# Kernel tuning notes

Measured on AMD Instinct MI355X. Metric: run time of the kernel, lower is better.

## Reference

```python
import jax, jax.numpy as jnp
import numpy as np

S, B, GL, OL = 512, 2048, 32, 20      # leaves: count, batch, genes, out
M, C, GM, OM = 32, 16, 64, 20         # mids: count, children, genes, out
GR, OR = 128, 38                      # root genes, root out
IM = C * OL + GM                      # 384 mid input
IR = M * OM + GR                      # 768 root input
EPS = 1e-5


def _bn(h, g, be, axis):
    # training-mode BatchNorm1d: biased batch variance, eps=1e-5
    m = h.mean(axis=axis, keepdims=True)
    v = h.var(axis=axis, keepdims=True)
    return g * (h - m) * jax.lax.rsqrt(v + EPS) + be


def setup_inputs() -> dict:
    key = jax.random.key(0)
    ks = jax.random.split(key, 8)
    d = {
        'x_leaf': jax.random.uniform(ks[0], (S, B, GL), dtype=jnp.float32),
        'x_mid': jax.random.uniform(ks[1], (M, B, GM), dtype=jnp.float32),
        'x_root': jax.random.uniform(ks[2], (B, GR), dtype=jnp.float32),
        'W_leaf': jax.random.normal(ks[3], (S, GL, OL), dtype=jnp.float32) * 0.1,
        'b_leaf': jnp.zeros((S, OL), jnp.float32),
        'g_leaf': jnp.ones((S, OL), jnp.float32),
        'be_leaf': jnp.zeros((S, OL), jnp.float32),
        'W_mid': jax.random.normal(ks[4], (M, IM, OM), dtype=jnp.float32) * 0.05,
        'b_mid': jnp.zeros((M, OM), jnp.float32),
        'g_mid': jnp.ones((M, OM), jnp.float32),
        'be_mid': jnp.zeros((M, OM), jnp.float32),
        'W_root': jax.random.normal(ks[5], (IR, OR), dtype=jnp.float32) * 0.05,
        'b_root': jnp.zeros((OR,), jnp.float32),
        'g_root': jnp.ones((OR,), jnp.float32),
        'be_root': jnp.zeros((OR,), jnp.float32),
    }
    return d


def reference(x_leaf, x_mid, x_root, W_leaf, b_leaf, g_leaf, be_leaf,
              W_mid, b_mid, g_mid, be_mid, W_root, b_root, g_root, be_root):
    # --- leaf subsystems (grouped GEMM over 512 subsystems) ---
    h = jnp.tanh(jnp.einsum('sbi,sio->sbo', x_leaf, W_leaf) + b_leaf[:, None, :])
    leaf_out = _bn(h, g_leaf[:, None, :], be_leaf[:, None, :], 1)  # [S,B,OL]
    # --- mid subsystems: concat(genes, child outputs) ---
    child = leaf_out.reshape(M, C, B, OL).transpose(0, 2, 1, 3).reshape(M, B, C * OL)
    xm = jnp.concatenate([x_mid, child], axis=-1)  # [M,B,IM]
    h = jnp.tanh(jnp.einsum('mbi,mio->mbo', xm, W_mid) + b_mid[:, None, :])
    mid_out = _bn(h, g_mid[:, None, :], be_mid[:, None, :], 1)  # [M,B,OM]
    # --- root subsystem ---
    childr = mid_out.transpose(1, 0, 2).reshape(B, M * OM)
    xr = jnp.concatenate([x_root, childr], axis=-1)  # [B,IR]
    h = jnp.tanh(xr @ W_root + b_root)
    return _bn(h, g_root, be_root, 0)  # [B,OR]
```

## Files before the change

kernel.cpp:

```cpp
#include <hip/hip_runtime.h>
#include <hip/hip_bf16.h>

#define SS 512
#define BATCH 2048
#define GL 32
#define OL 20
#define MM 32
#define CC 16
#define GM 64
#define OM 20
#define GR 128
#define ORR 38
#define IMID 384
#define IROOT 768
#define EPSBN 1e-5f

#define KSPLIT 16
#define KCH 48

#define SZ_CHILD ((size_t)SS * OL * BATCH)
#define OFF_SCL  (SZ_CHILD)
#define OFF_SHL  (OFF_SCL + (size_t)SS * OL)
#define OFF_HM   (OFF_SHL + (size_t)SS * OL)
#define OFF_MP   (OFF_HM + (size_t)MM * OM * BATCH)
#define OFF_HR   (OFF_MP + (size_t)MM * 32 * 2 * OM)
#define OFF_RP   (OFF_HR + (size_t)BATCH * ORR)
#define OFF_SCM  (OFF_RP + (size_t)32 * 76)
#define OFF_SHM  (OFF_SCM + (size_t)MM * OM)
#define OFF_PW   (OFF_SHM + (size_t)MM * OM)
#define OFF_LP   (OFF_PW + (size_t)KSPLIT * BATCH * ORR)

__device__ __forceinline__ float tanh_fast(float x) {
  float ax = fabsf(x);
  float e  = __expf(-2.0f * ax);
  float r  = __fdividef(1.0f - e, 1.0f + e);
  return copysignf(r, x);
}

__device__ __forceinline__ unsigned short f2bf(float f) {
  unsigned u = __builtin_bit_cast(unsigned, f);
  return (unsigned short)((u + 0x7FFFu + ((u >> 16) & 1u)) >> 16);
}

typedef __attribute__((ext_vector_type(8))) short short8v;
typedef __attribute__((ext_vector_type(4))) float f32x4;

#define FMA20(xs, wptr, acc) do { \
  const float4* _wr = (const float4*)(wptr); \
  float4 _w0=_wr[0], _w1=_wr[1], _w2=_wr[2], _w3=_wr[3], _w4=_wr[4]; \
  acc[0]=fmaf(xs,_w0.x,acc[0]);  acc[1]=fmaf(xs,_w0.y,acc[1]); \
  acc[2]=fmaf(xs,_w0.z,acc[2]);  acc[3]=fmaf(xs,_w0.w,acc[3]); \
  acc[4]=fmaf(xs,_w1.x,acc[4]);  acc[5]=fmaf(xs,_w1.y,acc[5]); \
  acc[6]=fmaf(xs,_w1.z,acc[6]);  acc[7]=fmaf(xs,_w1.w,acc[7]); \
  acc[8]=fmaf(xs,_w2.x,acc[8]);  acc[9]=fmaf(xs,_w2.y,acc[9]); \
  acc[10]=fmaf(xs,_w2.z,acc[10]); acc[11]=fmaf(xs,_w2.w,acc[11]); \
  acc[12]=fmaf(xs,_w3.x,acc[12]); acc[13]=fmaf(xs,_w3.y,acc[13]); \
  acc[14]=fmaf(xs,_w3.z,acc[14]); acc[15]=fmaf(xs,_w3.w,acc[15]); \
  acc[16]=fmaf(xs,_w4.x,acc[16]); acc[17]=fmaf(xs,_w4.y,acc[17]); \
  acc[18]=fmaf(xs,_w4.z,acc[18]); acc[19]=fmaf(xs,_w4.w,acc[19]); \
} while (0)

__global__ __launch_bounds__(256) void k_leaf(
    const float* __restrict__ x, const float* __restrict__ W,
    const float* __restrict__ bias, float* __restrict__ child,
    float* __restrict__ lp)
{
  const int chunk = blockIdx.x;
  const int s = blockIdx.y;
  const int t = threadIdx.x;
  const int w = t >> 6, l = t & 63;
  const int col = l & 15;
  const int kb = (l >> 4) * 8;

  __shared__ float hb[OL * 260];
  __shared__ float Wl[GL * OL];
  __shared__ float bl[OL];
  __shared__ float red[4][2 * OL];

  if (t < GL * OL / 4)
    ((float4*)Wl)[t] = ((const float4*)(W + (size_t)s * GL * OL))[t];
  else if (t >= 160 && t < 165)
    ((float4*)bl)[t - 160] = ((const float4*)(bias + s * OL))[t - 160];
  __syncthreads();

  short8v b0, b1;
#pragma unroll
  for (int j = 0; j < 8; j++) {
    const int k = kb + j;
    b0[j] = (short)f2bf(Wl[k * OL + col]);
    b1[j] = (col < 4) ? (short)f2bf(Wl[k * OL + 16 + col]) : (short)0;
  }
  const float blv0 = bl[col];
  const float blv1 = (col < 4) ? bl[16 + col] : 0.f;

  float sum0 = 0.f, ssq0 = 0.f, sum1 = 0.f, ssq1 = 0.f;
  const f32x4 zero = {0.f, 0.f, 0.f, 0.f};

#pragma unroll
  for (int T = 0; T < 4; T++) {
    const int tl = T * 64 + w * 16;
    const int row_g = chunk * 256 + tl + col;
    const float4* xr = (const float4*)(x + ((size_t)s * BATCH + row_g) * GL + kb);
    float4 v0 = xr[0], v1 = xr[1];
    short8v a;
    a[0] = (short)f2bf(v0.x); a[1] = (short)f2bf(v0.y);
    a[2] = (short)f2bf(v0.z); a[3] = (short)f2bf(v0.w);
    a[4] = (short)f2bf(v1.x); a[5] = (short)f2bf(v1.y);
    a[6] = (short)f2bf(v1.z); a[7] = (short)f2bf(v1.w);

    f32x4 d0 = __builtin_amdgcn_mfma_f32_16x16x32_bf16(a, b0, zero, 0, 0, 0);
    f32x4 d1 = __builtin_amdgcn_mfma_f32_16x16x32_bf16(a, b1, zero, 0, 0, 0);

    const int rowloc = tl + (l >> 4) * 4;
    float4 o0;
    o0.x = tanh_fast(d0[0] + blv0); o0.y = tanh_fast(d0[1] + blv0);
    o0.z = tanh_fast(d0[2] + blv0); o0.w = tanh_fast(d0[3] + blv0);
    sum0 += o0.x + o0.y + o0.z + o0.w;
    ssq0 = fmaf(o0.x, o0.x, fmaf(o0.y, o0.y, fmaf(o0.z, o0.z, fmaf(o0.w, o0.w, ssq0))));
    *(float4*)&hb[col * 260 + rowloc] = o0;
    if (col < 4) {
      float4 o1;
      o1.x = tanh_fast(d1[0] + blv1); o1.y = tanh_fast(d1[1] + blv1);
      o1.z = tanh_fast(d1[2] + blv1); o1.w = tanh_fast(d1[3] + blv1);
      sum1 += o1.x + o1.y + o1.z + o1.w;
      ssq1 = fmaf(o1.x, o1.x, fmaf(o1.y, o1.y, fmaf(o1.z, o1.z, fmaf(o1.w, o1.w, ssq1))));
      *(float4*)&hb[(16 + col) * 260 + rowloc] = o1;
    }
  }
  __syncthreads();

#pragma unroll
  for (int j = 0; j < 5; j++) {
    const int f = t + j * 256;
    const int plane = f >> 6, q = (f & 63) * 4;
    float4 v = *(const float4*)&hb[plane * 260 + q];
    *(float4*)&child[((size_t)s * OL + plane) * BATCH + chunk * 256 + q] = v;
  }

  sum0 += __shfl_xor(sum0, 16); sum0 += __shfl_xor(sum0, 32);
  ssq0 += __shfl_xor(ssq0, 16); ssq0 += __shfl_xor(ssq0, 32);
  sum1 += __shfl_xor(sum1, 16); sum1 += __shfl_xor(sum1, 32);
  ssq1 += __shfl_xor(ssq1, 16); ssq1 += __shfl_xor(ssq1, 32);
  if (l < 16) { red[w][l] = sum0; red[w][OL + l] = ssq0; }
  if (l < 4)  { red[w][16 + l] = sum1; red[w][OL + 16 + l] = ssq1; }
  __syncthreads();
  if (t < 2 * OL) {
    float v = red[0][t] + red[1][t] + red[2][t] + red[3][t];
    lp[((size_t)s * 8 + chunk) * (2 * OL) + t] = v;
  }
}

__global__ __launch_bounds__(256) void k_leafstats(
    const float* __restrict__ lp, const float* __restrict__ g,
    const float* __restrict__ be,
    float* __restrict__ scL, float* __restrict__ shL)
{
  const int e = blockIdx.x * 256 + threadIdx.x;
  if (e >= SS * OL) return;
  const int s = e / OL, o = e % OL;
  float s1 = 0.f, s2 = 0.f;
#pragma unroll
  for (int c = 0; c < 8; c++) {
    s1 += lp[((size_t)s * 8 + c) * (2 * OL) + o];
    s2 += lp[((size_t)s * 8 + c) * (2 * OL) + OL + o];
  }
  float mean = s1 * (1.f / BATCH);
  float var  = s2 * (1.f / BATCH) - mean * mean;
  float rs = rsqrtf(var + EPSBN);
  float sc = g[e] * rs;
  scL[e] = sc;
  shL[e] = be[e] - mean * sc;
}

__global__ __launch_bounds__(256, 2) void k_mid(
    const float* __restrict__ xg, const float* __restrict__ child,
    const float* __restrict__ scL, const float* __restrict__ shL,
    const float* __restrict__ W, const float* __restrict__ bias,
    float* __restrict__ hm, float* __restrict__ mp)
{
  const int chunk = blockIdx.x;
  const int m = blockIdx.y;
  const int t = threadIdx.x;
  const int kq = t >> 6;
  const int lane = t & 63;
  const int b = chunk * 64 + lane;

  __shared__ float Wl[IMID * OM];
  __shared__ float cb[3][64][21];
  __shared__ float scs[CC * OL];
  __shared__ float shs[CC * OL];
  __shared__ float xgb[64 * 69];

  for (int i = t; i < IMID * OM / 4; i += 256)
    ((float4*)Wl)[i] = ((const float4*)(W + (size_t)m * IMID * OM))[i];
  if (t < 80)       ((float4*)scs)[t]      = ((const float4*)(scL + m * CC * OL))[t];
  else if (t < 160) ((float4*)shs)[t - 80] = ((const float4*)(shL + m * CC * OL))[t - 80];

  {
    const float4* gs = (const float4*)(xg + ((size_t)m * BATCH + chunk * 64) * GM);
#pragma unroll
    for (int j = 0; j < 4; j++) {
      const int f = t + j * 256;
      float4 v = gs[f];
      const int r = f >> 4, c4 = (f & 15) << 2;
      float* wp = &xgb[r * 69 + c4];
      wp[0] = v.x; wp[1] = v.y; wp[2] = v.z; wp[3] = v.w;
    }
  }
  __syncthreads();

  float acc[OM];
#pragma unroll
  for (int o = 0; o < OM; o++) acc[o] = 0.f;

  const float* grow = &xgb[lane * 69 + kq * 16];
#pragma unroll
  for (int k = 0; k < 16; k++) {
    FMA20(grow[k], &Wl[(kq * 16 + k) * OM], acc);
  }
#pragma unroll 1
  for (int ci = 0; ci < 4; ci++) {
    const int c = kq * 4 + ci;
    const float* cbase = child + ((size_t)(m * CC + c) * OL) * BATCH + b;
#pragma unroll
    for (int o = 0; o < OL; o++) {
      float v = cbase[(size_t)o * BATCH];
      float xv = fmaf(v, scs[c * OL + o], shs[c * OL + o]);
      FMA20(xv, &Wl[(GM + c * OL + o) * OM], acc);
    }
  }

  if (kq > 0) {
#pragma unroll
    for (int o = 0; o < OM; o++) cb[kq - 1][lane][o] = acc[o];
  }
  __syncthreads();

  if (kq == 0) {
#pragma unroll
    for (int o = 0; o < OM; o++) {
      float v = acc[o] + cb[0][lane][o] + cb[1][lane][o] + cb[2][lane][o] + bias[m * OM + o];
      acc[o] = tanh_fast(v);
    }
#pragma unroll
    for (int o = 0; o < OM; o++)
      hm[((size_t)m * OM + o) * BATCH + b] = acc[o];
#pragma unroll
    for (int o = 0; o < OM; o++) {
      float s1 = acc[o], s2 = acc[o] * acc[o];
#pragma unroll
      for (int d = 32; d >= 1; d >>= 1) { s1 += __shfl_xor(s1, d); s2 += __shfl_xor(s2, d); }
      if (lane == 0) {
        mp[((size_t)m * 32 + chunk) * (2 * OM) + o] = s1;
        mp[((size_t)m * 32 + chunk) * (2 * OM) + OM + o] = s2;
      }
    }
  }
}

__global__ __launch_bounds__(256) void k_midstats(
    const float* __restrict__ mp, const float* __restrict__ g_mid,
    const float* __restrict__ be_mid,
    float* __restrict__ scm, float* __restrict__ shm)
{
  const int e = blockIdx.x * 256 + threadIdx.x;
  if (e >= MM * OM) return;
  const int m = e / OM, o = e % OM;
  float s1 = 0.f, s2 = 0.f;
  for (int c = 0; c < 32; c++) {
    s1 += mp[((size_t)m * 32 + c) * (2 * OM) + o];
    s2 += mp[((size_t)m * 32 + c) * (2 * OM) + OM + o];
  }
  float mean = s1 * (1.f / BATCH);
  float var  = s2 * (1.f / BATCH) - mean * mean;
  float r = rsqrtf(var + EPSBN);
  float sc = g_mid[e] * r;
  scm[e] = sc;
  shm[e] = be_mid[e] - mean * sc;
}

__global__ __launch_bounds__(256, 2) void k_root_partial(
    const float* __restrict__ xr, const float* __restrict__ hm,
    const float* __restrict__ scm, const float* __restrict__ shm,
    const float* __restrict__ W, float* __restrict__ pw)
{
  const int rc = blockIdx.x;
  const int kc = blockIdx.y;
  const int t = threadIdx.x;
  const int w = t >> 6, lane = t & 63;
  const int ob = w * 10;
  const bool full = (w < 3);
  const int b = rc * 64 + lane;
  const int k0 = kc * KCH;

  __shared__ float Wl[KCH * ORR];
  __shared__ float scs[KCH], shs[KCH];

  for (int i = t; i < KCH * ORR; i += 256)
    Wl[i] = W[(size_t)k0 * ORR + i];
  if (t < KCH) {
    const int mi = k0 + t - GR;
    const bool v = (mi >= 0);
    scs[t] = v ? scm[mi] : 0.f;
    shs[t] = v ? shm[mi] : 0.f;
  }
  __syncthreads();

  float acc[10];
#pragma unroll
  for (int j = 0; j < 10; j++) acc[j] = 0.f;

#define FMA10(xs, kk) do { \
    const float2* wr = (const float2*)(Wl + (size_t)(kk) * ORR + ob); \
    float2 w0 = wr[0], w1 = wr[1], w2 = wr[2], w3 = wr[3]; \
    float2 w4 = full ? wr[4] : make_float2(0.f, 0.f); \
    acc[0]=fmaf(xs,w0.x,acc[0]); acc[1]=fmaf(xs,w0.y,acc[1]); \
    acc[2]=fmaf(xs,w1.x,acc[2]); acc[3]=fmaf(xs,w1.y,acc[3]); \
    acc[4]=fmaf(xs,w2.x,acc[4]); acc[5]=fmaf(xs,w2.y,acc[5]); \
    acc[6]=fmaf(xs,w3.x,acc[6]); acc[7]=fmaf(xs,w3.y,acc[7]); \
    acc[8]=fmaf(xs,w4.x,acc[8]); acc[9]=fmaf(xs,w4.y,acc[9]); \
  } while (0)

#pragma unroll 2
  for (int g = 0; g < KCH / 4; g++) {
    const int k = k0 + g * 4;
    float xa[4];
    if (k < GR) {
      float4 xv = *(const float4*)(xr + (size_t)b * GR + k);
      xa[0] = xv.x; xa[1] = xv.y; xa[2] = xv.z; xa[3] = xv.w;
    } else {
      const int mi = k - GR;
      const float* hp = hm + (size_t)mi * BATCH + b;
      const int lk = g * 4;
#pragma unroll
      for (int j = 0; j < 4; j++)
        xa[j] = fmaf(hp[(size_t)j * BATCH], scs[lk + j], shs[lk + j]);
    }
#pragma unroll
    for (int j = 0; j < 4; j++) FMA10(xa[j], g * 4 + j);
  }
#undef FMA10

  const size_t base = ((size_t)kc * BATCH + b) * ORR + ob;
#pragma unroll
  for (int j = 0; j < 10; j++)
    if (j < 8 || full) pw[base + j] = acc[j];
}

__global__ __launch_bounds__(256) void k_rootfinal(
    const float* __restrict__ pw, const float* __restrict__ bias,
    float* __restrict__ hr, float* __restrict__ rp)
{
  const int blk = blockIdx.x;
  const int t = threadIdx.x;
  const int w = t >> 6, lane = t & 63;
  const int ob = w * 10;
  const bool full = (w < 3);
  const int b = blk * 64 + lane;

  float acc[10];
#pragma unroll
  for (int j = 0; j < 10; j++) acc[j] = 0.f;

#pragma unroll 1
  for (int kc = 0; kc < KSPLIT; kc++) {
    const size_t base = ((size_t)kc * BATCH + b) * ORR + ob;
#pragma unroll
    for (int j = 0; j < 10; j++)
      if (j < 8 || full) acc[j] += pw[base + j];
  }

#pragma unroll
  for (int j = 0; j < 10; j++) {
    float bj = (j < 8 || full) ? bias[ob + j] : 0.f;
    acc[j] = tanh_fast(acc[j] + bj);
  }

#pragma unroll
  for (int j = 0; j < 10; j++) {
    float s1 = acc[j], s2 = acc[j] * acc[j];
#pragma unroll
    for (int d = 32; d >= 1; d >>= 1) { s1 += __shfl_xor(s1, d); s2 += __shfl_xor(s2, d); }
    if (lane == 0 && (j < 8 || full)) {
      rp[blk * 76 + ob + j] = s1;
      rp[blk * 76 + ORR + ob + j] = s2;
    }
  }
#pragma unroll
  for (int j = 0; j < 10; j++)
    if (j < 8 || full) hr[(size_t)b * ORR + ob + j] = acc[j];
}

__global__ __launch_bounds__(256) void k_rootnorm(
    const float* __restrict__ hr, const float* __restrict__ rp,
    const float* __restrict__ g, const float* __restrict__ be,
    float* __restrict__ out)
{
  __shared__ float sc[ORR], sh[ORR];
  const int t = threadIdx.x;
  if (t < ORR) {
    float s1 = 0.f, s2 = 0.f;
    for (int blk = 0; blk < 32; blk++) {
      s1 += rp[blk * 76 + t];
      s2 += rp[blk * 76 + ORR + t];
    }
    float mean = s1 * (1.f / BATCH);
    float var  = s2 * (1.f / BATCH) - mean * mean;
    float r = rsqrtf(var + EPSBN);
    float scv = g[t] * r;
    sc[t] = scv;
    sh[t] = be[t] - mean * scv;
  }
  __syncthreads();
  const int idx = blockIdx.x * 256 + t;
  const int o = idx % ORR;
  out[idx] = hr[idx] * sc[o] + sh[o];
}

extern "C" void kernel_launch(void* const* d_in, const int* in_sizes, int n_in,
                              void* d_out, int out_size, void* d_ws, size_t ws_size,
                              hipStream_t stream) {
  (void)in_sizes; (void)n_in; (void)out_size; (void)ws_size;
  const float* x_leaf  = (const float*)d_in[0];
  const float* x_mid   = (const float*)d_in[1];
  const float* x_root  = (const float*)d_in[2];
  const float* W_leaf  = (const float*)d_in[3];
  const float* b_leaf  = (const float*)d_in[4];
  const float* g_leaf  = (const float*)d_in[5];
  const float* be_leaf = (const float*)d_in[6];
  const float* W_mid   = (const float*)d_in[7];
  const float* b_mid   = (const float*)d_in[8];
  const float* g_mid   = (const float*)d_in[9];
  const float* be_mid  = (const float*)d_in[10];
  const float* W_root  = (const float*)d_in[11];
  const float* b_root  = (const float*)d_in[12];
  const float* g_root  = (const float*)d_in[13];
  const float* be_root = (const float*)d_in[14];
  float* out = (float*)d_out;
  float* ws  = (float*)d_ws;

  float* child = ws;
  float* scL   = ws + OFF_SCL;
  float* shL   = ws + OFF_SHL;
  float* hm    = ws + OFF_HM;
  float* mp    = ws + OFF_MP;
  float* hr    = ws + OFF_HR;
  float* rp    = ws + OFF_RP;
  float* scm   = ws + OFF_SCM;
  float* shm   = ws + OFF_SHM;
  float* pw    = ws + OFF_PW;
  float* lp    = ws + OFF_LP;

  k_leaf<<<dim3(8, SS), 256, 0, stream>>>(x_leaf, W_leaf, b_leaf, child, lp);
  k_leafstats<<<40, 256, 0, stream>>>(lp, g_leaf, be_leaf, scL, shL);
  k_mid<<<dim3(32, MM), 256, 0, stream>>>(x_mid, child, scL, shL, W_mid, b_mid,
                                          hm, mp);
  k_midstats<<<3, 256, 0, stream>>>(mp, g_mid, be_mid, scm, shm);
  k_root_partial<<<dim3(32, KSPLIT), 256, 0, stream>>>(x_root, hm, scm, shm,
                                                       W_root, pw);
  k_rootfinal<<<32, 256, 0, stream>>>(pw, b_root, hr, rp);
  k_rootnorm<<<304, 256, 0, stream>>>(hr, rp, g_root, be_root, out);
}
```

Measured before the change: 128.0 us.

## Store leaf outputs and mid weights in bf16, read mid genes directly

Leaf activations are rounded to bf16 before being written to the intermediate child buffer, which halves the bytes written by the leaf kernel and read by the mid kernel. The mid weights are converted to packed bf16 pairs in shared memory, shrinking LDS usage, and the launch-bounds occupancy hint is dropped. Mid gene inputs are now read straight from global memory as float4 instead of being staged through shared memory. This trades accuracy for bandwidth: the leaf BN statistics are still computed from fp32 values, but the activations they normalise are bf16-rounded, and the weights also lose precision.

After: 208.3 us. 62.7% more time.

```diff
diff --git a/kernel.cpp b/kernel.cpp
--- a/kernel.cpp
+++ b/kernel.cpp
@@ -41,28 +41,31 @@
   unsigned u = __builtin_bit_cast(unsigned, f);
   return (unsigned short)((u + 0x7FFFu + ((u >> 16) & 1u)) >> 16);
 }
+__device__ __forceinline__ float bf2f(unsigned short u) {
+  return __builtin_bit_cast(float, ((unsigned)u) << 16);
+}
 
 typedef __attribute__((ext_vector_type(8))) short short8v;
 typedef __attribute__((ext_vector_type(4))) float f32x4;
 
-#define FMA20(xs, wptr, acc) do { \
-  const float4* _wr = (const float4*)(wptr); \
-  float4 _w0=_wr[0], _w1=_wr[1], _w2=_wr[2], _w3=_wr[3], _w4=_wr[4]; \
-  acc[0]=fmaf(xs,_w0.x,acc[0]);  acc[1]=fmaf(xs,_w0.y,acc[1]); \
-  acc[2]=fmaf(xs,_w0.z,acc[2]);  acc[3]=fmaf(xs,_w0.w,acc[3]); \
-  acc[4]=fmaf(xs,_w1.x,acc[4]);  acc[5]=fmaf(xs,_w1.y,acc[5]); \
-  acc[6]=fmaf(xs,_w1.z,acc[6]);  acc[7]=fmaf(xs,_w1.w,acc[7]); \
-  acc[8]=fmaf(xs,_w2.x,acc[8]);  acc[9]=fmaf(xs,_w2.y,acc[9]); \
-  acc[10]=fmaf(xs,_w2.z,acc[10]); acc[11]=fmaf(xs,_w2.w,acc[11]); \
-  acc[12]=fmaf(xs,_w3.x,acc[12]); acc[13]=fmaf(xs,_w3.y,acc[13]); \
-  acc[14]=fmaf(xs,_w3.z,acc[14]); acc[15]=fmaf(xs,_w3.w,acc[15]); \
-  acc[16]=fmaf(xs,_w4.x,acc[16]); acc[17]=fmaf(xs,_w4.y,acc[17]); \
-  acc[18]=fmaf(xs,_w4.z,acc[18]); acc[19]=fmaf(xs,_w4.w,acc[19]); \
+#define PKFMA(xs, u, a0, a1) do { \
+  a0 = fmaf(xs, __builtin_bit_cast(float, (unsigned)((u) << 16)), a0); \
+  a1 = fmaf(xs, __builtin_bit_cast(float, (unsigned)((u) & 0xFFFF0000u)), a1); \
+} while (0)
+
+#define FMA20P(xs, wp, acc) do { \
+  const uint4* _q = (const uint4*)(wp); \
+  uint4 _u0 = _q[0], _u1 = _q[1], _u2 = _q[2]; \
+  PKFMA(xs, _u0.x, acc[0], acc[1]);  PKFMA(xs, _u0.y, acc[2], acc[3]); \
+  PKFMA(xs, _u0.z, acc[4], acc[5]);  PKFMA(xs, _u0.w, acc[6], acc[7]); \
+  PKFMA(xs, _u1.x, acc[8], acc[9]);  PKFMA(xs, _u1.y, acc[10], acc[11]); \
+  PKFMA(xs, _u1.z, acc[12], acc[13]); PKFMA(xs, _u1.w, acc[14], acc[15]); \
+  PKFMA(xs, _u2.x, acc[16], acc[17]); PKFMA(xs, _u2.y, acc[18], acc[19]); \
 } while (0)
 
 __global__ __launch_bounds__(256) void k_leaf(
     const float* __restrict__ x, const float* __restrict__ W,
-    const float* __restrict__ bias, float* __restrict__ child,
+    const float* __restrict__ bias, unsigned short* __restrict__ child,
     float* __restrict__ lp)
 {
   const int chunk = blockIdx.x;
@@ -134,7 +137,9 @@
     const int f = t + j * 256;
     const int plane = f >> 6, q = (f & 63) * 4;
     float4 v = *(const float4*)&hb[plane * 260 + q];
-    *(float4*)&child[((size_t)s * OL + plane) * BATCH + chunk * 256 + q] = v;
+    ushort4 p;
+    p.x = f2bf(v.x); p.y = f2bf(v.y); p.z = f2bf(v.z); p.w = f2bf(v.w);
+    *(ushort4*)&child[((size_t)s * OL + plane) * BATCH + chunk * 256 + q] = p;
   }
 
   sum0 += __shfl_xor(sum0, 16); sum0 += __shfl_xor(sum0, 32);
@@ -172,8 +177,8 @@
   shL[e] = be[e] - mean * sc;
 }
 
-__global__ __launch_bounds__(256, 2) void k_mid(
-    const float* __restrict__ xg, const float* __restrict__ child,
+__global__ __launch_bounds__(256) void k_mid(
+    const float* __restrict__ xg, const unsigned short* __restrict__ child,
     const float* __restrict__ scL, const float* __restrict__ shL,
     const float* __restrict__ W, const float* __restrict__ bias,
     float* __restrict__ hm, float* __restrict__ mp)
@@ -185,48 +190,43 @@
   const int lane = t & 63;
   const int b = chunk * 64 + lane;
 
-  __shared__ float Wl[IMID * OM];
+  __shared__ unsigned Wp[IMID * 12];
   __shared__ float cb[3][64][21];
   __shared__ float scs[CC * OL];
   __shared__ float shs[CC * OL];
-  __shared__ float xgb[64 * 69];
-
-  for (int i = t; i < IMID * OM / 4; i += 256)
-    ((float4*)Wl)[i] = ((const float4*)(W + (size_t)m * IMID * OM))[i];
+
+  for (int i = t; i < IMID * 10; i += 256) {
+    const int k = i / 10, j = i - k * 10;
+    const float* wsrc = W + (size_t)m * IMID * OM + k * OM + j * 2;
+    Wp[k * 12 + j] = ((unsigned)f2bf(wsrc[0])) | (((unsigned)f2bf(wsrc[1])) << 16);
+  }
   if (t < 80)       ((float4*)scs)[t]      = ((const float4*)(scL + m * CC * OL))[t];
   else if (t < 160) ((float4*)shs)[t - 80] = ((const float4*)(shL + m * CC * OL))[t - 80];
-
-  {
-    const float4* gs = (const float4*)(xg + ((size_t)m * BATCH + chunk * 64) * GM);
-#pragma unroll
-    for (int j = 0; j < 4; j++) {
-      const int f = t + j * 256;
-      float4 v = gs[f];
-      const int r = f >> 4, c4 = (f & 15) << 2;
-      float* wp = &xgb[r * 69 + c4];
-      wp[0] = v.x; wp[1] = v.y; wp[2] = v.z; wp[3] = v.w;
-    }
-  }
   __syncthreads();
 
   float acc[OM];
 #pragma unroll
   for (int o = 0; o < OM; o++) acc[o] = 0.f;
 
-  const float* grow = &xgb[lane * 69 + kq * 16];
-#pragma unroll
-  for (int k = 0; k < 16; k++) {
-    FMA20(grow[k], &Wl[(kq * 16 + k) * OM], acc);
+  const float4* gx = (const float4*)(xg + ((size_t)m * BATCH + b) * GM + kq * 16);
+#pragma unroll
+  for (int j4 = 0; j4 < 4; j4++) {
+    float4 xv = gx[j4];
+    const int k = kq * 16 + j4 * 4;
+    FMA20P(xv.x, &Wp[(k + 0) * 12], acc);
+    FMA20P(xv.y, &Wp[(k + 1) * 12], acc);
+    FMA20P(xv.z, &Wp[(k + 2) * 12], acc);
+    FMA20P(xv.w, &Wp[(k + 3) * 12], acc);
   }
 #pragma unroll 1
   for (int ci = 0; ci < 4; ci++) {
     const int c = kq * 4 + ci;
-    const float* cbase = child + ((size_t)(m * CC + c) * OL) * BATCH + b;
+    const unsigned short* cbase = child + ((size_t)(m * CC + c) * OL) * BATCH + b;
 #pragma unroll
     for (int o = 0; o < OL; o++) {
-      float v = cbase[(size_t)o * BATCH];
+      float v = bf2f(cbase[(size_t)o * BATCH]);
       float xv = fmaf(v, scs[c * OL + o], shs[c * OL + o]);
-      FMA20(xv, &Wl[(GM + c * OL + o) * OM], acc);
+      FMA20P(xv, &Wp[(GM + c * OL + o) * 12], acc);
     }
   }
 
@@ -439,7 +439,7 @@
   float* out = (float*)d_out;
   float* ws  = (float*)d_ws;
 
-  float* child = ws;
+  unsigned short* child = (unsigned short*)ws;
   float* scL   = ws + OFF_SCL;
   float* shL   = ws + OFF_SHL;
   float* hm    = ws + OFF_HM;
```

## Rewrite mid-level GEMM on bf16 MFMA with split-precision child inputs and folded BN

Applied to the files above, without the earlier changes.

Replaces the scalar FP32 FMA loop in the mid-subsystem kernel with 16x16x32 bf16 MFMA instructions. The leaf BatchNorm scale is folded into the weights and the shift into an adjusted bias. Child activations are split into hi and lo bf16 parts to keep accuracy. Outputs are staged through LDS for coalesced float4 stores, and statistics are reduced with shuffles. The cost is per-block weight conversion overhead, doubled MFMA work on the child part, and a loss of precision from bf16 weights.

After: 106.8 us, median of 2. -16.6%, faster.

```diff
diff --git a/kernel.cpp b/kernel.cpp
--- a/kernel.cpp
+++ b/kernel.cpp
@@ -41,24 +41,12 @@
   unsigned u = __builtin_bit_cast(unsigned, f);
   return (unsigned short)((u + 0x7FFFu + ((u >> 16) & 1u)) >> 16);
 }
+__device__ __forceinline__ float bf2f(unsigned short u) {
+  return __builtin_bit_cast(float, ((unsigned)u) << 16);
+}
 
 typedef __attribute__((ext_vector_type(8))) short short8v;
 typedef __attribute__((ext_vector_type(4))) float f32x4;
-
-#define FMA20(xs, wptr, acc) do { \
-  const float4* _wr = (const float4*)(wptr); \
-  float4 _w0=_wr[0], _w1=_wr[1], _w2=_wr[2], _w3=_wr[3], _w4=_wr[4]; \
-  acc[0]=fmaf(xs,_w0.x,acc[0]);  acc[1]=fmaf(xs,_w0.y,acc[1]); \
-  acc[2]=fmaf(xs,_w0.z,acc[2]);  acc[3]=fmaf(xs,_w0.w,acc[3]); \
-  acc[4]=fmaf(xs,_w1.x,acc[4]);  acc[5]=fmaf(xs,_w1.y,acc[5]); \
-  acc[6]=fmaf(xs,_w1.z,acc[6]);  acc[7]=fmaf(xs,_w1.w,acc[7]); \
-  acc[8]=fmaf(xs,_w2.x,acc[8]);  acc[9]=fmaf(xs,_w2.y,acc[9]); \
-  acc[10]=fmaf(xs,_w2.z,acc[10]); acc[11]=fmaf(xs,_w2.w,acc[11]); \
-  acc[12]=fmaf(xs,_w3.x,acc[12]); acc[13]=fmaf(xs,_w3.y,acc[13]); \
-  acc[14]=fmaf(xs,_w3.z,acc[14]); acc[15]=fmaf(xs,_w3.w,acc[15]); \
-  acc[16]=fmaf(xs,_w4.x,acc[16]); acc[17]=fmaf(xs,_w4.y,acc[17]); \
-  acc[18]=fmaf(xs,_w4.z,acc[18]); acc[19]=fmaf(xs,_w4.w,acc[19]); \
-} while (0)
 
 __global__ __launch_bounds__(256) void k_leaf(
     const float* __restrict__ x, const float* __restrict__ W,
@@ -172,7 +160,7 @@
   shL[e] = be[e] - mean * sc;
 }
 
-__global__ __launch_bounds__(256, 2) void k_mid(
+__global__ __launch_bounds__(256) void k_mid(
     const float* __restrict__ xg, const float* __restrict__ child,
     const float* __restrict__ scL, const float* __restrict__ shL,
     const float* __restrict__ W, const float* __restrict__ bias,
@@ -181,80 +169,142 @@
   const int chunk = blockIdx.x;
   const int m = blockIdx.y;
   const int t = threadIdx.x;
-  const int kq = t >> 6;
-  const int lane = t & 63;
-  const int b = chunk * 64 + lane;
-
-  __shared__ float Wl[IMID * OM];
-  __shared__ float cb[3][64][21];
-  __shared__ float scs[CC * OL];
-  __shared__ float shs[CC * OL];
-  __shared__ float xgb[64 * 69];
-
-  for (int i = t; i < IMID * OM / 4; i += 256)
-    ((float4*)Wl)[i] = ((const float4*)(W + (size_t)m * IMID * OM))[i];
+  const int w = t >> 6, l = t & 63;
+  const int col = l & 15;
+  const int kb = (l >> 4) * 8;
+
+  __shared__ short bfr[12 * 2 * 64 * 8];
+  __shared__ float ovl[1360];
+  __shared__ float red[4][2 * OM];
+  __shared__ float bias2[OM];
+
+  float* scs = ovl;
+  float* shs = ovl + 320;
+  float* part = ovl + 640;
+  float* hb = ovl;
+
+  const float* Wm = W + (size_t)m * IMID * OM;
+
   if (t < 80)       ((float4*)scs)[t]      = ((const float4*)(scL + m * CC * OL))[t];
   else if (t < 160) ((float4*)shs)[t - 80] = ((const float4*)(shL + m * CC * OL))[t - 80];
-
+  __syncthreads();
+
+#pragma unroll 1
+  for (int i = 0; i < 48; i++) {
+    const int e = t + i * 256;
+    const int kt = e >> 10;
+    const int ct = (e >> 9) & 1;
+    const int ll = (e >> 3) & 63;
+    const int j = e & 7;
+    const int k = kt * 32 + (ll >> 4) * 8 + j;
+    const int n = ct * 16 + (ll & 15);
+    float val = 0.f;
+    if (n < OM) {
+      float wv = Wm[k * OM + n];
+      val = (k < GM) ? wv : scs[k - GM] * wv;
+    }
+    bfr[e] = (short)f2bf(val);
+  }
+  if (t < 160) {
+    const int n = t >> 3, p = t & 7;
+    const int fb = p * 40;
+    float sacc = 0.f;
+#pragma unroll 1
+    for (int f = 0; f < 40; f++)
+      sacc = fmaf(shs[fb + f], Wm[(GM + fb + f) * OM + n], sacc);
+    part[t] = sacc;
+  }
+  __syncthreads();
+  if (t < OM) {
+    float sb = bias[m * OM + t];
+#pragma unroll
+    for (int p = 0; p < 8; p++) sb += part[t * 8 + p];
+    bias2[t] = sb;
+  }
+  __syncthreads();
+
+  const int row = chunk * 64 + w * 16 + col;
+  f32x4 acc0 = {0.f, 0.f, 0.f, 0.f};
+  f32x4 acc1 = {0.f, 0.f, 0.f, 0.f};
+
+#pragma unroll
+  for (int kt = 0; kt < 2; kt++) {
+    const float4* gp = (const float4*)(xg + ((size_t)m * BATCH + row) * GM + kt * 32 + kb);
+    float4 v0 = gp[0], v1 = gp[1];
+    short8v a;
+    a[0] = (short)f2bf(v0.x); a[1] = (short)f2bf(v0.y);
+    a[2] = (short)f2bf(v0.z); a[3] = (short)f2bf(v0.w);
+    a[4] = (short)f2bf(v1.x); a[5] = (short)f2bf(v1.y);
+    a[6] = (short)f2bf(v1.z); a[7] = (short)f2bf(v1.w);
+    short8v bf0 = *(const short8v*)&bfr[kt * 1024 + l * 8];
+    short8v bf1 = *(const short8v*)&bfr[kt * 1024 + 512 + l * 8];
+    acc0 = __builtin_amdgcn_mfma_f32_16x16x32_bf16(a, bf0, acc0, 0, 0, 0);
+    acc1 = __builtin_amdgcn_mfma_f32_16x16x32_bf16(a, bf1, acc1, 0, 0, 0);
+  }
+#pragma unroll 1
+  for (int kt = 2; kt < 12; kt++) {
+    const float* cp = child + ((size_t)m * (CC * OL) + (kt - 2) * 32 + kb) * BATCH + row;
+    short8v ah, al;
+#pragma unroll
+    for (int j = 0; j < 8; j++) {
+      float v = cp[(size_t)j * BATCH];
+      unsigned short hi = f2bf(v);
+      ah[j] = (short)hi;
+      al[j] = (short)f2bf(v - bf2f(hi));
+    }
+    short8v bf0 = *(const short8v*)&bfr[kt * 1024 + l * 8];
+    short8v bf1 = *(const short8v*)&bfr[kt * 1024 + 512 + l * 8];
+    acc0 = __builtin_amdgcn_mfma_f32_16x16x32_bf16(ah, bf0, acc0, 0, 0, 0);
+    acc0 = __builtin_amdgcn_mfma_f32_16x16x32_bf16(al, bf0, acc0, 0, 0, 0);
+    acc1 = __builtin_amdgcn_mfma_f32_16x16x32_bf16(ah, bf1, acc1, 0, 0, 0);
+    acc1 = __builtin_amdgcn_mfma_f32_16x16x32_bf16(al, bf1, acc1, 0, 0, 0);
+  }
+
+  const float bv0 = bias2[col];
+  const float bv1 = (col < 4) ? bias2[16 + col] : 0.f;
+  const int rowloc = w * 16 + (l >> 4) * 4;
+  float sum0, ssq0, sum1 = 0.f, ssq1 = 0.f;
   {
-    const float4* gs = (const float4*)(xg + ((size_t)m * BATCH + chunk * 64) * GM);
-#pragma unroll
-    for (int j = 0; j < 4; j++) {
-      const int f = t + j * 256;
-      float4 v = gs[f];
-      const int r = f >> 4, c4 = (f & 15) << 2;
-      float* wp = &xgb[r * 69 + c4];
-      wp[0] = v.x; wp[1] = v.y; wp[2] = v.z; wp[3] = v.w;
-    }
-  }
-  __syncthreads();
-
-  float acc[OM];
-#pragma unroll
-  for (int o = 0; o < OM; o++) acc[o] = 0.f;
-
-  const float* grow = &xgb[lane * 69 + kq * 16];
-#pragma unroll
-  for (int k = 0; k < 16; k++) {
-    FMA20(grow[k], &Wl[(kq * 16 + k) * OM], acc);
-  }
-#pragma unroll 1
-  for (int ci = 0; ci < 4; ci++) {
-    const int c = kq * 4 + ci;
-    const float* cbase = child + ((size_t)(m * CC + c) * OL) * BATCH + b;
-#pragma unroll
-    for (int o = 0; o < OL; o++) {
-      float v = cbase[(size_t)o * BATCH];
-      float xv = fmaf(v, scs[c * OL + o], shs[c * OL + o]);
-      FMA20(xv, &Wl[(GM + c * OL + o) * OM], acc);
-    }
-  }
-
-  if (kq > 0) {
-#pragma unroll
-    for (int o = 0; o < OM; o++) cb[kq - 1][lane][o] = acc[o];
-  }
-  __syncthreads();
-
-  if (kq == 0) {
-#pragma unroll
-    for (int o = 0; o < OM; o++) {
-      float v = acc[o] + cb[0][lane][o] + cb[1][lane][o] + cb[2][lane][o] + bias[m * OM + o];
-      acc[o] = tanh_fast(v);
-    }
-#pragma unroll
-    for (int o = 0; o < OM; o++)
-      hm[((size_t)m * OM + o) * BATCH + b] = acc[o];
-#pragma unroll
-    for (int o = 0; o < OM; o++) {
-      float s1 = acc[o], s2 = acc[o] * acc[o];
-#pragma unroll
-      for (int d = 32; d >= 1; d >>= 1) { s1 += __shfl_xor(s1, d); s2 += __shfl_xor(s2, d); }
-      if (lane == 0) {
-        mp[((size_t)m * 32 + chunk) * (2 * OM) + o] = s1;
-        mp[((size_t)m * 32 + chunk) * (2 * OM) + OM + o] = s2;
-      }
-    }
+    float4 o0;
+    o0.x = tanh_fast(acc0[0] + bv0); o0.y = tanh_fast(acc0[1] + bv0);
+    o0.z = tanh_fast(acc0[2] + bv0); o0.w = tanh_fast(acc0[3] + bv0);
+    sum0 = o0.x + o0.y + o0.z + o0.w;
+    ssq0 = fmaf(o0.x, o0.x, fmaf(o0.y, o0.y, fmaf(o0.z, o0.z, o0.w * o0.w)));
+    *(float4*)&hb[col * 68 + rowloc] = o0;
+    if (col < 4) {
+      float4 o1;
+      o1.x = tanh_fast(acc1[0] + bv1); o1.y = tanh_fast(acc1[1] + bv1);
+      o1.z = tanh_fast(acc1[2] + bv1); o1.w = tanh_fast(acc1[3] + bv1);
+      sum1 = o1.x + o1.y + o1.z + o1.w;
+      ssq1 = fmaf(o1.x, o1.x, fmaf(o1.y, o1.y, fmaf(o1.z, o1.z, o1.w * o1.w)));
+      *(float4*)&hb[(16 + col) * 68 + rowloc] = o1;
+    }
+  }
+  __syncthreads();
+
+  {
+    const int f = t;
+    const int plane = f >> 4, q = (f & 15) * 4;
+    float4 v = *(const float4*)&hb[plane * 68 + q];
+    *(float4*)&hm[((size_t)m * OM + plane) * BATCH + chunk * 64 + q] = v;
+  }
+  if (t < 64) {
+    const int f = t + 256;
+    const int plane = f >> 4, q = (f & 15) * 4;
+    float4 v = *(const float4*)&hb[plane * 68 + q];
+    *(float4*)&hm[((size_t)m * OM + plane) * BATCH + chunk * 64 + q] = v;
+  }
+
+  sum0 += __shfl_xor(sum0, 16); sum0 += __shfl_xor(sum0, 32);
+  ssq0 += __shfl_xor(ssq0, 16); ssq0 += __shfl_xor(ssq0, 32);
+  sum1 += __shfl_xor(sum1, 16); sum1 += __shfl_xor(sum1, 32);
+  ssq1 += __shfl_xor(ssq1, 16); ssq1 += __shfl_xor(ssq1, 32);
+  if (l < 16) { red[w][l] = sum0; red[w][OM + l] = ssq0; }
+  if (l < 4)  { red[w][16 + l] = sum1; red[w][OM + 16 + l] = ssq1; }
+  __syncthreads();
+  if (t < 2 * OM) {
+    float v = red[0][t] + red[1][t] + red[2][t] + red[3][t];
+    mp[((size_t)m * 32 + chunk) * (2 * OM) + t] = v;
   }
 }
 
```
